# Performance work log

Measured on AMD Instinct MI355X. Metric: run time of the kernel, lower is better.

The kernel has to match this reference:

```python
import jax, jax.numpy as jnp
import numpy as np

N_Q = 4  # n_qubits == hidden_dim


def _qgate(z, phi):
    # Quantum circuit closed form: all gates are single-qubit RX, so the state is a
    # product state. Wires 0,1 get RX(z[:,w]) encoding then trainable RX(phi[w]);
    # wires >=2 get only trainable RX(phi[w]). <PauliZ> after RX(theta)|0> = cos(theta).
    B = z.shape[0]
    ang01 = z[:, :2] + phi[:2]                                  # [B, 2]
    ang_rest = jnp.broadcast_to(phi[2:], (B, N_Q - 2))          # [B, N_Q-2]
    return jnp.cos(jnp.concatenate([ang01, ang_rest], axis=1))  # [B, N_Q]


def setup_inputs() -> dict:
    key = jax.random.key(0)
    ks = jax.random.split(key, 13)
    T, B, D, H = 512, 256, 256, N_Q
    s = 0.1
    inp = {"inputs": jax.random.normal(ks[0], (T, B, D), dtype=jnp.float32)}
    for j, n in enumerate(["f", "i", "u", "o"]):
        inp["W" + n] = jax.random.normal(ks[1 + 3 * j], (H, D + H), dtype=jnp.float32) * s
        inp["b" + n] = jax.random.normal(ks[2 + 3 * j], (H,), dtype=jnp.float32) * s
        inp["phi_" + n] = jax.random.normal(ks[3 + 3 * j], (H,), dtype=jnp.float32) * s
    return inp


def reference(inputs, Wf, bf, phi_f, Wi, bi, phi_i, Wu, bu, phi_u, Wo, bo, phi_o):
    B = inputs.shape[1]
    H = Wf.shape[0]

    def step(carry, x):
        hx, cx = carry
        c = jnp.concatenate([x, hx], axis=1)                     # [B, D+H]
        f = jax.nn.sigmoid(_qgate(c @ Wf.T + bf, phi_f))
        i = jax.nn.sigmoid(_qgate(c @ Wi.T + bi, phi_i))
        g = jnp.tanh(_qgate(c @ Wu.T + bu, phi_u))
        o = jax.nn.sigmoid(_qgate(c @ Wo.T + bo, phi_o))
        cx_new = f * cx + i * g
        hx_new = o * jnp.tanh(cx_new)
        return (hx_new, cx_new), hx_new

    h0 = jnp.zeros((B, H), inputs.dtype)
    c0 = jnp.zeros((B, H), inputs.dtype)
    (hx, cx), outputs = jax.lax.scan(step, (h0, c0), inputs)
    return outputs, hx, cx
```

## Files before the change

kernel.cpp:

```cpp
#include <hip/hip_runtime.h>
#include <math.h>

#define TT 512
#define BB 256
#define DD 256
#define INV2PI 0.15915494309189535f
#define CHUNK 32
#define WARM 24
#define NCH (TT / CHUNK)

typedef float v2f __attribute__((ext_vector_type(2)));
typedef float v4f __attribute__((ext_vector_type(4)));

__device__ __forceinline__ v2f pkfma(v2f a, v2f b, v2f c) {
    return __builtin_elementwise_fma(a, b, c);
}
__device__ __forceinline__ v2f cos2(v2f a) {
    v2f r;
    r.x = __builtin_amdgcn_cosf(a.x);
    r.y = __builtin_amdgcn_cosf(a.y);
    return r;
}
__device__ __forceinline__ v2f sig2(v2f x) {
    v2f u = x * x;
    v2f p = pkfma(u, (v2f)(-2.1081349e-4f), (v2f)(2.0833333e-3f));
    p = pkfma(u, p, (v2f)(-2.0833333e-2f));
    p = pkfma(u, p, (v2f)(0.25f));
    return pkfma(x, p, (v2f)(0.5f));
}
__device__ __forceinline__ v2f tanh2(v2f x) {
    v2f u = x * x;
    v2f n = pkfma(u + (v2f)(105.0f), u, (v2f)(945.0f));
    v2f d = pkfma(pkfma(u, (v2f)(15.0f), (v2f)(420.0f)), u, (v2f)(945.0f));
    v2f r;
    r.x = __builtin_amdgcn_rcpf(d.x);
    r.y = __builtin_amdgcn_rcpf(d.y);
    return x * n * r;
}

__device__ __forceinline__ float reduce8(float p[8], int lane) {
    const bool b0 = lane & 1;
#pragma unroll
    for (int k = 0; k < 4; ++k) {
        float send = b0 ? p[k] : p[k + 4];
        float q = __shfl_xor(send, 1, 64);
        p[k] = (b0 ? p[k + 4] : p[k]) + q;
    }
    const bool b1 = lane & 2;
#pragma unroll
    for (int k = 0; k < 2; ++k) {
        float send = b1 ? p[k] : p[k + 2];
        float q = __shfl_xor(send, 2, 64);
        p[k] = (b1 ? p[k + 2] : p[k]) + q;
    }
    const bool b2 = lane & 4;
    {
        float send = b2 ? p[0] : p[1];
        float q = __shfl_xor(send, 4, 64);
        p[0] = (b2 ? p[1] : p[0]) + q;
    }
    p[0] += __shfl_xor(p[0], 8, 64);
    p[0] += __shfl_xor(p[0], 16, 64);
    p[0] += __shfl_xor(p[0], 32, 64);
    return p[0];
}

__global__ __launch_bounds__(256) void qlstm_setup(
    const float* __restrict__ Wf, const float* __restrict__ bf, const float* __restrict__ pf,
    const float* __restrict__ Wi, const float* __restrict__ bi, const float* __restrict__ pi,
    const float* __restrict__ Wu, const float* __restrict__ bu, const float* __restrict__ pu,
    const float* __restrict__ Wo, const float* __restrict__ bo, const float* __restrict__ po,
    float* __restrict__ hcf, float* __restrict__ hob) {
    const int tid = threadIdx.x;
    const float* Ws[4] = {Wf, Wi, Wu, Wo};
    const float* Bs[4] = {bf, bi, bu, bo};
    const float* Ps[4] = {pf, pi, pu, po};

    float l2fc[2], Scc[2], occ[2], ricc[2];
#pragma unroll
    for (int w = 0; w < 2; ++w) {
        const int q = w + 2;
        float fv = 1.0f / (1.0f + expf(-cosf(Ps[0][q])));
        float iv = 1.0f / (1.0f + expf(-cosf(Ps[1][q])));
        float gv = tanhf(cosf(Ps[2][q]));
        float ov = 1.0f / (1.0f + expf(-cosf(Ps[3][q])));
        l2fc[w] = log2f(fv);
        Scc[w] = iv * gv;
        occ[w] = ov;
        ricc[w] = 1.0f / (1.0f - fv);
    }
    float bb[8];
#pragma unroll
    for (int g = 0; g < 4; ++g)
#pragma unroll
        for (int wire = 0; wire < 2; ++wire) bb[g * 2 + wire] = Bs[g][wire] + Ps[g][wire];

    for (int t = tid; t < TT; t += 256) {
        float h2 = occ[0] * tanhf(Scc[0] * (1.0f - exp2f((float)t * l2fc[0])) * ricc[0]);
        float h3 = occ[1] * tanhf(Scc[1] * (1.0f - exp2f((float)t * l2fc[1])) * ricc[1]);
        float ho2 = occ[0] * tanhf(Scc[0] * (1.0f - exp2f((float)(t + 1) * l2fc[0])) * ricc[0]);
        float ho3 = occ[1] * tanhf(Scc[1] * (1.0f - exp2f((float)(t + 1) * l2fc[1])) * ricc[1]);
#pragma unroll
        for (int g = 0; g < 4; ++g)
#pragma unroll
            for (int wire = 0; wire < 2; ++wire)
                hcf[t * 8 + g * 2 + wire] =
                    (bb[g * 2 + wire] + h2 * Ws[g][wire * 260 + 258] + h3 * Ws[g][wire * 260 + 259]) * INV2PI;
        hob[t * 2] = ho2;
        hob[t * 2 + 1] = ho3;
    }
}

__global__ __launch_bounds__(256) void qlstm_gemm(
    const float* __restrict__ x,
    const float* __restrict__ Wf, const float* __restrict__ Wi,
    const float* __restrict__ Wu, const float* __restrict__ Wo,
    const float* __restrict__ hcf, const float* __restrict__ hob,
    float* __restrict__ Z, float* __restrict__ out) {
    const int tid = threadIdx.x;
    const int lane = tid & 63;
    const int wid = (blockIdx.x * 256 + tid) >> 6;
    const int tbase = wid >> 8;
    const float* Ws[4] = {Wf, Wi, Wu, Wo};

    float4 wv[8];
#pragma unroll
    for (int g = 0; g < 4; ++g)
#pragma unroll
        for (int wire = 0; wire < 2; ++wire)
            wv[g * 2 + wire] = *(const float4*)(Ws[g] + wire * 260 + 4 * lane);
    const int v = ((lane & 1) << 2) | (lane & 2) | ((lane >> 2) & 1);

    v4f xcur[4], xnxt[4];
#pragma unroll
    for (int j = 0; j < 4; ++j)
        xcur[j] = *(const v4f*)(x + (size_t)(wid + j * 8192) * DD + 4 * lane);

#pragma unroll
    for (int k = 0; k < 16; k += 4) {
        float hv[4];
        float2 hb;
        if (lane < 8) {
#pragma unroll
            for (int j = 0; j < 4; ++j) hv[j] = hcf[(tbase + (k + j) * 32) * 8 + v];
        } else if (lane < 12) {
            hb = *(const float2*)(hob + (tbase + (k + lane - 8) * 32) * 2);
        }
        if (k < 12) {
#pragma unroll
            for (int j = 0; j < 4; ++j)
                xnxt[j] = *(const v4f*)(x + (size_t)(wid + (k + 4 + j) * 8192) * DD + 4 * lane);
        }
#pragma unroll
        for (int j = 0; j < 4; ++j) {
            float p[8];
#pragma unroll
            for (int m = 0; m < 8; ++m)
                p[m] = xcur[j].x * wv[m].x + xcur[j].y * wv[m].y + xcur[j].z * wv[m].z +
                       xcur[j].w * wv[m].w;
            float s = reduce8(p, lane);
            if (lane < 8)
                Z[(size_t)(wid + (k + j) * 8192) * 8 + v] = s * INV2PI + hv[j];
        }
        if (lane >= 8 && lane < 12)
            *(float2*)(out + (size_t)(wid + (k + lane - 8) * 8192) * 4 + 2) = hb;
        if (k < 12) {
#pragma unroll
            for (int j = 0; j < 4; ++j) xcur[j] = xnxt[j];
        }
    }
}

__global__ __launch_bounds__(64) void qlstm_scan(
    const float* __restrict__ Z,
    const float* __restrict__ Wf, const float* __restrict__ pf,
    const float* __restrict__ Wi, const float* __restrict__ pi,
    const float* __restrict__ Wu, const float* __restrict__ pu,
    const float* __restrict__ Wo, const float* __restrict__ po,
    float* __restrict__ out) {
    const int tid = threadIdx.x;
    const int chunk = blockIdx.x >> 2;
    const int b = (blockIdx.x & 3) * 64 + tid;
    const float* Ws[4] = {Wf, Wi, Wu, Wo};
    const float* Ps[4] = {pf, pi, pu, po};

    float cd[2], hd[2];
#pragma unroll
    for (int w = 0; w < 2; ++w) {
        const int q = w + 2;
        float fv = 1.0f / (1.0f + expf(-cosf(Ps[0][q])));
        float iv = 1.0f / (1.0f + expf(-cosf(Ps[1][q])));
        float gv = tanhf(cosf(Ps[2][q]));
        float ov = 1.0f / (1.0f + expf(-cosf(Ps[3][q])));
        float l2f = log2f(fv);
        float S = iv * gv;
        float ric = 1.0f / (1.0f - fv);
        cd[w] = S * (1.0f - exp2f(512.0f * l2f)) * ric;
        hd[w] = ov * tanhf(cd[w]);
    }

    v2f wa[4], wb[4];
#pragma unroll
    for (int g = 0; g < 4; ++g) {
        wa[g].x = Ws[g][256] * INV2PI;
        wa[g].y = Ws[g][260 + 256] * INV2PI;
        wb[g].x = Ws[g][257] * INV2PI;
        wb[g].y = Ws[g][260 + 257] * INV2PI;
    }

    const int t0 = chunk * CHUNK;
    const int tw = (t0 - WARM > 0) ? (t0 - WARM) : 0;
    const int len = t0 + CHUNK - tw;

    v2f h = (v2f)(0.0f), c = (v2f)(0.0f);
    const float* Zb = Z + (size_t)b * 8;
    float* outp = out + (size_t)b * 4;
    v4f zbuf[8][2];
#pragma unroll
    for (int s = 0; s < 8; ++s) {
        zbuf[s][0] = *(const v4f*)(Zb + (size_t)(tw + s) * 2048);
        zbuf[s][1] = *(const v4f*)(Zb + (size_t)(tw + s) * 2048 + 4);
    }

#pragma unroll 8
    for (int s = 0; s < len; ++s) {
        const int t = tw + s;
        const int slot = s & 7;
        v4f zA = zbuf[slot][0], zB = zbuf[slot][1];
        if (s + 8 < len) {
            zbuf[slot][0] = *(const v4f*)(Zb + (size_t)(t + 8) * 2048);
            zbuf[slot][1] = *(const v4f*)(Zb + (size_t)(t + 8) * 2048 + 4);
        }
        v2f zf = {zA.x, zA.y}, zi = {zA.z, zA.w}, zu = {zB.x, zB.y}, zo = {zB.z, zB.w};
        v2f h0s = (v2f)(h.x), h1s = (v2f)(h.y);
        v2f af = pkfma(h0s, wa[0], pkfma(h1s, wb[0], zf));
        v2f ai = pkfma(h0s, wa[1], pkfma(h1s, wb[1], zi));
        v2f au = pkfma(h0s, wa[2], pkfma(h1s, wb[2], zu));
        v2f ao = pkfma(h0s, wa[3], pkfma(h1s, wb[3], zo));
        v2f f = sig2(cos2(af));
        v2f i = sig2(cos2(ai));
        v2f g = tanh2(cos2(au));
        v2f o = sig2(cos2(ao));
        c = pkfma(f, c, i * g);
        v2f th = tanh2(c);
        h = o * th;
        if (t >= t0)
            *(v2f*)(outp + (size_t)t * (BB * 4)) = h;
    }

    if (chunk == NCH - 1) {
        *(float4*)(out + (size_t)TT * BB * 4 + (size_t)b * 4) =
            make_float4(h.x, h.y, hd[0], hd[1]);
        *(float4*)(out + (size_t)TT * BB * 4 + (size_t)BB * 4 + (size_t)b * 4) =
            make_float4(c.x, c.y, cd[0], cd[1]);
    }
}

extern "C" void kernel_launch(void* const* d_in, const int* in_sizes, int n_in,
                              void* d_out, int out_size, void* d_ws, size_t ws_size,
                              hipStream_t stream) {
    (void)in_sizes; (void)n_in; (void)out_size; (void)ws_size;
    const float* x  = (const float*)d_in[0];
    const float* Wf = (const float*)d_in[1];
    const float* bf = (const float*)d_in[2];
    const float* pf = (const float*)d_in[3];
    const float* Wi = (const float*)d_in[4];
    const float* bi = (const float*)d_in[5];
    const float* pi = (const float*)d_in[6];
    const float* Wu = (const float*)d_in[7];
    const float* bu = (const float*)d_in[8];
    const float* pu = (const float*)d_in[9];
    const float* Wo = (const float*)d_in[10];
    const float* bo = (const float*)d_in[11];
    const float* po = (const float*)d_in[12];
    float* out = (float*)d_out;
    float* Z = (float*)d_ws;
    float* hcf = Z + (size_t)TT * BB * 8;
    float* hob = hcf + (size_t)TT * 8;

    qlstm_setup<<<1, 256, 0, stream>>>(Wf, bf, pf, Wi, bi, pi, Wu, bu, pu,
                                       Wo, bo, po, hcf, hob);
    qlstm_gemm<<<2048, 256, 0, stream>>>(x, Wf, Wi, Wu, Wo, hcf, hob, Z, out);
    qlstm_scan<<<NCH * 4, 64, 0, stream>>>(Z, Wf, pf, Wi, pi, Wu, pu, Wo, po, out);
}
```

Before: 237.0 us.

## Fold setup kernel into scan, computing bias/constant-wire terms in shared memory

Removes the single-block setup kernel and computes the per-timestep bias and constant-wire hidden terms inside each scan block, storing them in shared memory. The scan adds those terms to Z and writes the constant hidden outputs alongside h as one 16-byte store. The gemm kernel drops the hcf/hob loads and the strided output writes. This saves one launch and a serialized tiny kernel, but adds setup work and a barrier at the start of each scan block and extra LDS reads inside the latency-bound recurrence.

Result: no change. 233.0 us (-1.7%).

```diff
diff --git a/kernel.cpp b/kernel.cpp
--- a/kernel.cpp
+++ b/kernel.cpp
@@ -8,6 +8,7 @@
 #define CHUNK 32
 #define WARM 24
 #define NCH (TT / CHUNK)
+#define MAXLEN (CHUNK + WARM)
 
 typedef float v2f __attribute__((ext_vector_type(2)));
 typedef float v4f __attribute__((ext_vector_type(4)));
@@ -65,18 +66,75 @@
     return p[0];
 }
 
-__global__ __launch_bounds__(256) void qlstm_setup(
+__global__ __launch_bounds__(256) void qlstm_gemm(
+    const float* __restrict__ x,
+    const float* __restrict__ Wf, const float* __restrict__ Wi,
+    const float* __restrict__ Wu, const float* __restrict__ Wo,
+    float* __restrict__ Z) {
+    const int tid = threadIdx.x;
+    const int lane = tid & 63;
+    const int wid = (blockIdx.x * 256 + tid) >> 6;
+    const float* Ws[4] = {Wf, Wi, Wu, Wo};
+
+    float4 wv[8];
+#pragma unroll
+    for (int g = 0; g < 4; ++g)
+#pragma unroll
+        for (int wire = 0; wire < 2; ++wire)
+            wv[g * 2 + wire] = *(const float4*)(Ws[g] + wire * 260 + 4 * lane);
+    const int v = ((lane & 1) << 2) | (lane & 2) | ((lane >> 2) & 1);
+
+    v4f xcur[4], xnxt[4];
+#pragma unroll
+    for (int j = 0; j < 4; ++j)
+        xcur[j] = *(const v4f*)(x + (size_t)(wid + j * 8192) * DD + 4 * lane);
+
+#pragma unroll
+    for (int k = 0; k < 16; k += 4) {
+        if (k < 12) {
+#pragma unroll
+            for (int j = 0; j < 4; ++j)
+                xnxt[j] = *(const v4f*)(x + (size_t)(wid + (k + 4 + j) * 8192) * DD + 4 * lane);
+        }
+#pragma unroll
+        for (int j = 0; j < 4; ++j) {
+            float p[8];
+#pragma unroll
+            for (int m = 0; m < 8; ++m)
+                p[m] = xcur[j].x * wv[m].x + xcur[j].y * wv[m].y + xcur[j].z * wv[m].z +
+                       xcur[j].w * wv[m].w;
+            float s = reduce8(p, lane);
+            if (lane < 8)
+                Z[(size_t)(wid + (k + j) * 8192) * 8 + v] = s * INV2PI;
+        }
+        if (k < 12) {
+#pragma unroll
+            for (int j = 0; j < 4; ++j) xcur[j] = xnxt[j];
+        }
+    }
+}
+
+__global__ __launch_bounds__(64) void qlstm_scan(
+    const float* __restrict__ Z,
     const float* __restrict__ Wf, const float* __restrict__ bf, const float* __restrict__ pf,
     const float* __restrict__ Wi, const float* __restrict__ bi, const float* __restrict__ pi,
     const float* __restrict__ Wu, const float* __restrict__ bu, const float* __restrict__ pu,
     const float* __restrict__ Wo, const float* __restrict__ bo, const float* __restrict__ po,
-    float* __restrict__ hcf, float* __restrict__ hob) {
+    float* __restrict__ out) {
+    __shared__ float hcf_s[MAXLEN * 8];
+    __shared__ float hob_s[MAXLEN * 2];
     const int tid = threadIdx.x;
+    const int chunk = blockIdx.x >> 2;
+    const int b = (blockIdx.x & 3) * 64 + tid;
     const float* Ws[4] = {Wf, Wi, Wu, Wo};
     const float* Bs[4] = {bf, bi, bu, bo};
     const float* Ps[4] = {pf, pi, pu, po};
 
-    float l2fc[2], Scc[2], occ[2], ricc[2];
+    const int t0 = chunk * CHUNK;
+    const int tw = (t0 - WARM > 0) ? (t0 - WARM) : 0;
+    const int len = t0 + CHUNK - tw;
+
+    float l2fc[2], Scc[2], occ2[2], ricc[2];
 #pragma unroll
     for (int w = 0; w < 2; ++w) {
         const int q = w + 2;
@@ -86,117 +144,30 @@
         float ov = 1.0f / (1.0f + expf(-cosf(Ps[3][q])));
         l2fc[w] = log2f(fv);
         Scc[w] = iv * gv;
-        occ[w] = ov;
+        occ2[w] = ov;
         ricc[w] = 1.0f / (1.0f - fv);
     }
-    float bb[8];
-#pragma unroll
-    for (int g = 0; g < 4; ++g)
-#pragma unroll
-        for (int wire = 0; wire < 2; ++wire) bb[g * 2 + wire] = Bs[g][wire] + Ps[g][wire];
-
-    for (int t = tid; t < TT; t += 256) {
-        float h2 = occ[0] * tanhf(Scc[0] * (1.0f - exp2f((float)t * l2fc[0])) * ricc[0]);
-        float h3 = occ[1] * tanhf(Scc[1] * (1.0f - exp2f((float)t * l2fc[1])) * ricc[1]);
-        float ho2 = occ[0] * tanhf(Scc[0] * (1.0f - exp2f((float)(t + 1) * l2fc[0])) * ricc[0]);
-        float ho3 = occ[1] * tanhf(Scc[1] * (1.0f - exp2f((float)(t + 1) * l2fc[1])) * ricc[1]);
+    float cd[2], hd[2];
+#pragma unroll
+    for (int w = 0; w < 2; ++w) {
+        cd[w] = Scc[w] * (1.0f - exp2f(512.0f * l2fc[w])) * ricc[w];
+        hd[w] = occ2[w] * tanhf(cd[w]);
+    }
+    if (tid < len) {
+        const int t = tw + tid;
+        float h2 = occ2[0] * tanhf(Scc[0] * (1.0f - exp2f((float)t * l2fc[0])) * ricc[0]);
+        float h3 = occ2[1] * tanhf(Scc[1] * (1.0f - exp2f((float)t * l2fc[1])) * ricc[1]);
+        float ho2 = occ2[0] * tanhf(Scc[0] * (1.0f - exp2f((float)(t + 1) * l2fc[0])) * ricc[0]);
+        float ho3 = occ2[1] * tanhf(Scc[1] * (1.0f - exp2f((float)(t + 1) * l2fc[1])) * ricc[1]);
 #pragma unroll
         for (int g = 0; g < 4; ++g)
 #pragma unroll
             for (int wire = 0; wire < 2; ++wire)
-                hcf[t * 8 + g * 2 + wire] =
-                    (bb[g * 2 + wire] + h2 * Ws[g][wire * 260 + 258] + h3 * Ws[g][wire * 260 + 259]) * INV2PI;
-        hob[t * 2] = ho2;
-        hob[t * 2 + 1] = ho3;
-    }
-}
-
-__global__ __launch_bounds__(256) void qlstm_gemm(
-    const float* __restrict__ x,
-    const float* __restrict__ Wf, const float* __restrict__ Wi,
-    const float* __restrict__ Wu, const float* __restrict__ Wo,
-    const float* __restrict__ hcf, const float* __restrict__ hob,
-    float* __restrict__ Z, float* __restrict__ out) {
-    const int tid = threadIdx.x;
-    const int lane = tid & 63;
-    const int wid = (blockIdx.x * 256 + tid) >> 6;
-    const int tbase = wid >> 8;
-    const float* Ws[4] = {Wf, Wi, Wu, Wo};
-
-    float4 wv[8];
-#pragma unroll
-    for (int g = 0; g < 4; ++g)
-#pragma unroll
-        for (int wire = 0; wire < 2; ++wire)
-            wv[g * 2 + wire] = *(const float4*)(Ws[g] + wire * 260 + 4 * lane);
-    const int v = ((lane & 1) << 2) | (lane & 2) | ((lane >> 2) & 1);
-
-    v4f xcur[4], xnxt[4];
-#pragma unroll
-    for (int j = 0; j < 4; ++j)
-        xcur[j] = *(const v4f*)(x + (size_t)(wid + j * 8192) * DD + 4 * lane);
-
-#pragma unroll
-    for (int k = 0; k < 16; k += 4) {
-        float hv[4];
-        float2 hb;
-        if (lane < 8) {
-#pragma unroll
-            for (int j = 0; j < 4; ++j) hv[j] = hcf[(tbase + (k + j) * 32) * 8 + v];
-        } else if (lane < 12) {
-            hb = *(const float2*)(hob + (tbase + (k + lane - 8) * 32) * 2);
-        }
-        if (k < 12) {
-#pragma unroll
-            for (int j = 0; j < 4; ++j)
-                xnxt[j] = *(const v4f*)(x + (size_t)(wid + (k + 4 + j) * 8192) * DD + 4 * lane);
-        }
-#pragma unroll
-        for (int j = 0; j < 4; ++j) {
-            float p[8];
-#pragma unroll
-            for (int m = 0; m < 8; ++m)
-                p[m] = xcur[j].x * wv[m].x + xcur[j].y * wv[m].y + xcur[j].z * wv[m].z +
-                       xcur[j].w * wv[m].w;
-            float s = reduce8(p, lane);
-            if (lane < 8)
-                Z[(size_t)(wid + (k + j) * 8192) * 8 + v] = s * INV2PI + hv[j];
-        }
-        if (lane >= 8 && lane < 12)
-            *(float2*)(out + (size_t)(wid + (k + lane - 8) * 8192) * 4 + 2) = hb;
-        if (k < 12) {
-#pragma unroll
-            for (int j = 0; j < 4; ++j) xcur[j] = xnxt[j];
-        }
-    }
-}
-
-__global__ __launch_bounds__(64) void qlstm_scan(
-    const float* __restrict__ Z,
-    const float* __restrict__ Wf, const float* __restrict__ pf,
-    const float* __restrict__ Wi, const float* __restrict__ pi,
-    const float* __restrict__ Wu, const float* __restrict__ pu,
-    const float* __restrict__ Wo, const float* __restrict__ po,
-    float* __restrict__ out) {
-    const int tid = threadIdx.x;
-    const int chunk = blockIdx.x >> 2;
-    const int b = (blockIdx.x & 3) * 64 + tid;
-    const float* Ws[4] = {Wf, Wi, Wu, Wo};
-    const float* Ps[4] = {pf, pi, pu, po};
-
-    float cd[2], hd[2];
-#pragma unroll
-    for (int w = 0; w < 2; ++w) {
-        const int q = w + 2;
-        float fv = 1.0f / (1.0f + expf(-cosf(Ps[0][q])));
-        float iv = 1.0f / (1.0f + expf(-cosf(Ps[1][q])));
-        float gv = tanhf(cosf(Ps[2][q]));
-        float ov = 1.0f / (1.0f + expf(-cosf(Ps[3][q])));
-        float l2f = log2f(fv);
-        float S = iv * gv;
-        float ric = 1.0f / (1.0f - fv);
-        cd[w] = S * (1.0f - exp2f(512.0f * l2f)) * ric;
-        hd[w] = ov * tanhf(cd[w]);
+                hcf_s[tid * 8 + g * 2 + wire] =
+                    (Bs[g][wire] + Ps[g][wire] + h2 * Ws[g][wire * 260 + 258] +
+                     h3 * Ws[g][wire * 260 + 259]) * INV2PI;
+        hob_s[tid * 2] = ho2;
+        hob_s[tid * 2 + 1] = ho3;
     }
 
     v2f wa[4], wb[4];
@@ -208,9 +179,7 @@
         wb[g].y = Ws[g][260 + 257] * INV2PI;
     }
 
-    const int t0 = chunk * CHUNK;
-    const int tw = (t0 - WARM > 0) ? (t0 - WARM) : 0;
-    const int len = t0 + CHUNK - tw;
+    __syncthreads();
 
     v2f h = (v2f)(0.0f), c = (v2f)(0.0f);
     const float* Zb = Z + (size_t)b * 8;
@@ -231,7 +200,12 @@
             zbuf[slot][0] = *(const v4f*)(Zb + (size_t)(t + 8) * 2048);
             zbuf[slot][1] = *(const v4f*)(Zb + (size_t)(t + 8) * 2048 + 4);
         }
+        v2f hcf_f = *(const v2f*)&hcf_s[s * 8 + 0];
+        v2f hcf_i = *(const v2f*)&hcf_s[s * 8 + 2];
+        v2f hcf_u = *(const v2f*)&hcf_s[s * 8 + 4];
+        v2f hcf_o = *(const v2f*)&hcf_s[s * 8 + 6];
         v2f zf = {zA.x, zA.y}, zi = {zA.z, zA.w}, zu = {zB.x, zB.y}, zo = {zB.z, zB.w};
+        zf += hcf_f; zi += hcf_i; zu += hcf_u; zo += hcf_o;
         v2f h0s = (v2f)(h.x), h1s = (v2f)(h.y);
         v2f af = pkfma(h0s, wa[0], pkfma(h1s, wb[0], zf));
         v2f ai = pkfma(h0s, wa[1], pkfma(h1s, wb[1], zi));
@@ -244,8 +218,14 @@
         c = pkfma(f, c, i * g);
         v2f th = tanh2(c);
         h = o * th;
-        if (t >= t0)
-            *(v2f*)(outp + (size_t)t * (BB * 4)) = h;
+        if (t >= t0) {
+            v4f o4;
+            o4.x = h.x;
+            o4.y = h.y;
+            o4.z = hob_s[s * 2];
+            o4.w = hob_s[s * 2 + 1];
+            *(v4f*)(outp + (size_t)t * (BB * 4)) = o4;
+        }
     }
 
     if (chunk == NCH - 1) {
@@ -275,11 +255,8 @@
     const float* po = (const float*)d_in[12];
     float* out = (float*)d_out;
     float* Z = (float*)d_ws;
-    float* hcf = Z + (size_t)TT * BB * 8;
-    float* hob = hcf + (size_t)TT * 8;
-
-    qlstm_setup<<<1, 256, 0, stream>>>(Wf, bf, pf, Wi, bi, pi, Wu, bu, pu,
-                                       Wo, bo, po, hcf, hob);
-    qlstm_gemm<<<2048, 256, 0, stream>>>(x, Wf, Wi, Wu, Wo, hcf, hob, Z, out);
-    qlstm_scan<<<NCH * 4, 64, 0, stream>>>(Z, Wf, pf, Wi, pi, Wu, pu, Wo, po, out);
-}
+
+    qlstm_gemm<<<2048, 256, 0, stream>>>(x, Wf, Wi, Wu, Wo, Z);
+    qlstm_scan<<<NCH * 4, 64, 0, stream>>>(Z, Wf, bf, pf, Wi, bi, pi, Wu, bu, pu,
+                                           Wo, bo, po, out);
+}
```
